# Performance work log

Hardware: AMD Instinct MI355X
Metric: run time of the kernel (lower is better)

## Reference

```python
import jax, jax.numpy as jnp
import numpy as np

B, S, E, H = 4, 2048, 1024, 16
DK = E // H  # 64


def setup_inputs() -> dict:
    key = jax.random.key(0)
    ks = jax.random.split(key, 12)
    sc_in = 1.0 / np.sqrt(E)
    sc_dk = 1.0 / np.sqrt(DK)
    inp = {
        "Q": jax.random.normal(ks[0], (B, S, E), jnp.float32),
        "K": jax.random.normal(ks[1], (B, S, E), jnp.float32),
        "V": jax.random.normal(ks[2], (B, S, E), jnp.float32),
        # per-head projection weights, torch Linear layout [out, in] stacked over heads
        "Wq": jax.random.normal(ks[3], (H, DK, E), jnp.float32) * sc_in,
        "bq": jax.random.normal(ks[4], (H, DK), jnp.float32) * sc_in,
        "Wk": jax.random.normal(ks[5], (H, DK, E), jnp.float32) * sc_in,
        "bk": jax.random.normal(ks[6], (H, DK), jnp.float32) * sc_in,
        "Wv": jax.random.normal(ks[7], (H, DK, E), jnp.float32) * sc_in,
        "bv": jax.random.normal(ks[8], (H, DK), jnp.float32) * sc_in,
        # output projection (intended embed_dim -> embed_dim)
        "Wo": jax.random.normal(ks[9], (E, E), jnp.float32) * sc_in,
        "bo": jax.random.normal(ks[10], (E,), jnp.float32) * sc_in,
    }
    return inp


def reference(Q, K, V, Wq, bq, Wk, bk, Wv, bv, Wo, bo):
    scale = 1.0 / jnp.sqrt(jnp.asarray(DK, Q.dtype))
    # per-head linear projections (vectorized over heads): [B,H,S,DK]
    q = jnp.einsum("bse,hde->bhsd", Q, Wq) + bq[None, :, None, :]
    k = jnp.einsum("bse,hde->bhsd", K, Wk) + bk[None, :, None, :]
    v = jnp.einsum("bse,hde->bhsd", V, Wv) + bv[None, :, None, :]
    # scaled dot-product attention (no mask, dropout=0.0)
    scores = jnp.einsum("bhsd,bhtd->bhst", q, k) * scale  # [B,H,S,S]
    attn = jax.nn.softmax(scores, axis=-1)
    ctx = jnp.einsum("bhst,bhtd->bhsd", attn, v)  # [B,H,S,DK]
    # concat heads along feature dim -> [B,S,E]
    ctx = ctx.transpose(0, 2, 1, 3).reshape(B, S, E)
    return ctx @ Wo.T + bo
```

## Files before the change

kernel.cpp:

```cpp
#include <hip/hip_runtime.h>
#include <stdint.h>

typedef __attribute__((ext_vector_type(8))) short vs8;
typedef __attribute__((ext_vector_type(4))) short vs4;
typedef __attribute__((ext_vector_type(4))) float vf4;

#define DEV static __device__ __forceinline__

DEV unsigned short f2bf(float x){
  union { float f; uint32_t u; } v; v.f = x;
  uint32_t r = v.u + 0x7fffu + ((v.u >> 16) & 1u);
  return (unsigned short)(r >> 16);
}

DEV void gload_lds16(const void* g, void* l){
  __builtin_amdgcn_global_load_lds((const __attribute__((address_space(1))) void*)g,
                                   (__attribute__((address_space(3))) void*)l, 16, 0, 0);
}

DEV int cvtpk(float lo, float hi_){
  int r; asm("v_cvt_pk_bf16_f32 %0, %1, %2" : "=v"(r) : "v"(lo), "v"(hi_)); return r;
}

__global__ void cvt_w(const float* __restrict__ s, unsigned short* __restrict__ d, int n){
  int i = (blockIdx.x * blockDim.x + threadIdx.x) * 4;
  if (i >= n) return;
  vf4 f = *reinterpret_cast<const vf4*>(s + i);
  vs4 o;
  o[0] = (short)f2bf(f[0]); o[1] = (short)f2bf(f[1]);
  o[2] = (short)f2bf(f[2]); o[3] = (short)f2bf(f[3]);
  *reinterpret_cast<vs4*>(d + i) = o;
}


DEV void stage_bf16(const unsigned short* __restrict__ g, long row0, int K, int kt,
                    unsigned short* lds, int lane, int wid){
#pragma unroll
  for (int i = 0; i < 4; ++i){
    int stripe = wid*32 + i*8;
    int row = stripe + (lane >> 3);
    int chunk = (lane & 7) ^ (row & 7);
    const unsigned short* src = g + (row0 + row) * (long)K + kt + chunk*8;
    gload_lds16(src, &lds[stripe*64]);
  }
}

DEV vs8 lds_frag(const unsigned short* lds, int row, int slot){
  return *reinterpret_cast<const vs8*>(&lds[row*64 + (slot ^ (row & 7))*8]);
}

template<int OUT_F32, int BIAS_ROW>
__global__ __launch_bounds__(256)
void gemm_bt(const unsigned short* __restrict__ Ap, const unsigned short* __restrict__ Bp,
             const float* __restrict__ bias, void* __restrict__ Cp,
             int M, int N, int K, float oscale, long aB, long bB, long cB)
{
  __shared__ unsigned short As[128*64];
  __shared__ unsigned short Bs[128*64];
  const int tid = threadIdx.x, lane = tid & 63, wid = tid >> 6;
  const int nt = N >> 7, mt = M >> 7;
  int idx = blockIdx.x;
  const int per = mt * nt;
  const int batch = idx / per; idx -= batch * per;
  const long m0 = (long)(idx / nt) * 128;
  const long n0 = (long)(idx % nt) * 128;
  const int wm = (wid >> 1) * 64, wn = (wid & 1) * 64;
  const int cl = lane & 15, gr = lane >> 4;

  vf4 acc[4][4] = {};

  for (int kt = 0; kt < K; kt += 64){
    stage_bf16(Ap + aB*batch, m0, K, kt, As, lane, wid);
    stage_bf16(Bp + bB*batch, n0, K, kt, Bs, lane, wid);
    __syncthreads();
#pragma unroll
    for (int ks = 0; ks < 2; ++ks){
      vs8 af[4], bf[4];
#pragma unroll
      for (int mi = 0; mi < 4; ++mi) af[mi] = lds_frag(As, wm + mi*16 + cl, ks*4 + gr);
#pragma unroll
      for (int ni = 0; ni < 4; ++ni) bf[ni] = lds_frag(Bs, wn + ni*16 + cl, ks*4 + gr);
#pragma unroll
      for (int mi = 0; mi < 4; ++mi)
#pragma unroll
        for (int ni = 0; ni < 4; ++ni)
          acc[mi][ni] = __builtin_amdgcn_mfma_f32_16x16x32_bf16(af[mi], bf[ni], acc[mi][ni], 0, 0, 0);
    }
    __syncthreads();
  }

#pragma unroll
  for (int mi = 0; mi < 4; ++mi)
#pragma unroll
    for (int ni = 0; ni < 4; ++ni)
#pragma unroll
      for (int r = 0; r < 4; ++r){
        long m = m0 + wm + mi*16 + gr*4 + r;
        long n = n0 + wn + ni*16 + cl;
        float v = (acc[mi][ni][r] + (BIAS_ROW ? bias[m] : bias[n])) * oscale;
        if (OUT_F32) (((float*)Cp) + cB*batch)[m*(long)N + n] = v;
        else (((unsigned short*)Cp) + cB*batch)[m*(long)N + n] = f2bf(v);
      }
}

__global__ __launch_bounds__(256)
void attn_kernel(const unsigned short* __restrict__ qg, const unsigned short* __restrict__ kg,
                 const unsigned short* __restrict__ vg, unsigned short* __restrict__ og)
{
  __shared__ __align__(16) unsigned short Ks[2][64*64];
  __shared__ __align__(16) unsigned short Vs[2][8*64*8];
  __shared__ __align__(16) unsigned short Pl[4][16*72];
  const int tid = threadIdx.x, lane = tid & 63, wid = tid >> 6;
  const int cl = lane & 15, gr = lane >> 4;
  const int bid = blockIdx.x;
  const int qb = bid & 31, h = (bid >> 5) & 15, b = bid >> 9;
  const int s0 = qb*64 + wid*16;

  const unsigned short* qp = qg + ((long)(b*2048 + s0 + cl))*1024 + h*64 + gr*8;
  vs8 q0 = *(const vs8*)(qp);
  vs8 q1 = *(const vs8*)(qp + 32);

  const unsigned short* kb = kg + ((long)b*2048)*1024 + h*64;
  const unsigned short* vb = vg + ((long)(b*1024) + h*64)*2048;

  vf4 o0 = {}, o1 = {}, o2 = {}, o3 = {};
  float m = -__builtin_inff(), lsum = 0.f;

  const int krow = tid >> 3;
  const int kchunk = ((tid & 7) ^ (krow & 7)) * 8;
  const int vd = tid >> 2, vsl = tid & 3;
  const int kbase = (tid & 192) * 8;
  unsigned short* Pw = Pl[wid];

  gload_lds16(kb + (long)krow*1024 + kchunk,        &Ks[0][kbase]);
  gload_lds16(kb + (long)(krow + 32)*1024 + kchunk, &Ks[0][32*64 + kbase]);
  {
    vs8 va = *(const vs8*)(vb + (long)vd*2048 + vsl*8);
    vs8 vb2 = *(const vs8*)(vb + (long)vd*2048 + 32 + vsl*8);
    *(vs8*)(&Vs[0][(vsl*64 + vd)*8]) = va;
    *(vs8*)(&Vs[0][((vsl + 4)*64 + vd)*8]) = vb2;
  }
  __syncthreads();

  int cur = 0;
  for (int j0 = 0; j0 < 2048; j0 += 64){
    const int more = (j0 + 64) < 2048;
    vs8 va, vb2;
    if (more){
      const long nj = j0 + 64;
      gload_lds16(kb + (nj + krow)*1024 + kchunk,      &Ks[cur ^ 1][kbase]);
      gload_lds16(kb + (nj + krow + 32)*1024 + kchunk, &Ks[cur ^ 1][32*64 + kbase]);
      va  = *(const vs8*)(vb + (long)vd*2048 + nj + vsl*8);
      vb2 = *(const vs8*)(vb + (long)vd*2048 + nj + 32 + vsl*8);
    }
    const unsigned short* ksb = Ks[cur];
    const unsigned short* vsb = Vs[cur];

    vf4 s[4];
#pragma unroll
    for (int jt = 0; jt < 4; ++jt){
      vf4 z = {};
      vs8 aA = lds_frag(ksb, jt*16 + cl, gr);
      z = __builtin_amdgcn_mfma_f32_16x16x32_bf16(aA, q0, z, 0, 0, 0);
      vs8 aB = lds_frag(ksb, jt*16 + cl, 4 + gr);
      z = __builtin_amdgcn_mfma_f32_16x16x32_bf16(aB, q1, z, 0, 0, 0);
      s[jt] = z;
    }

    float t0 = fmaxf(fmaxf(s[0][0], s[0][1]), fmaxf(s[0][2], s[0][3]));
    float t1 = fmaxf(fmaxf(s[1][0], s[1][1]), fmaxf(s[1][2], s[1][3]));
    float t2 = fmaxf(fmaxf(s[2][0], s[2][1]), fmaxf(s[2][2], s[2][3]));
    float t3 = fmaxf(fmaxf(s[3][0], s[3][1]), fmaxf(s[3][2], s[3][3]));
    float t = fmaxf(fmaxf(t0, t1), fmaxf(t2, t3));
    t = fmaxf(t, __shfl_xor(t, 16));
    t = fmaxf(t, __shfl_xor(t, 32));

    if (__any(t > m + 8.f)){
      float mn = fmaxf(m, t);
      float al = __builtin_amdgcn_exp2f(m - mn);
      m = mn; lsum *= al;
#pragma unroll
      for (int r = 0; r < 4; ++r){ o0[r] *= al; o1[r] *= al; o2[r] *= al; o3[r] *= al; }
    }

#pragma unroll
    for (int jt = 0; jt < 4; ++jt)
#pragma unroll
      for (int r = 0; r < 4; ++r)
        s[jt][r] = __builtin_amdgcn_exp2f(s[jt][r] - m);
    lsum += (((s[0][0]+s[0][1]) + (s[0][2]+s[0][3])) + ((s[1][0]+s[1][1]) + (s[1][2]+s[1][3])))
          + (((s[2][0]+s[2][1]) + (s[2][2]+s[2][3])) + ((s[3][0]+s[3][1]) + (s[3][2]+s[3][3])));

#pragma unroll
    for (int jt = 0; jt < 4; ++jt){
      int2 w;
      w.x = cvtpk(s[jt][0], s[jt][1]);
      w.y = cvtpk(s[jt][2], s[jt][3]);
      *reinterpret_cast<int2*>(&Pw[cl*72 + jt*16 + gr*4]) = w;
    }
    vs8 pa0 = *reinterpret_cast<const vs8*>(&Pw[cl*72 + gr*8]);
    vs8 pa1 = *reinterpret_cast<const vs8*>(&Pw[cl*72 + 32 + gr*8]);

    o0 = __builtin_amdgcn_mfma_f32_16x16x32_bf16(*(const vs8*)(vsb + (gr*64 +  0 + cl)*8), pa0, o0, 0, 0, 0);
    o1 = __builtin_amdgcn_mfma_f32_16x16x32_bf16(*(const vs8*)(vsb + (gr*64 + 16 + cl)*8), pa0, o1, 0, 0, 0);
    o2 = __builtin_amdgcn_mfma_f32_16x16x32_bf16(*(const vs8*)(vsb + (gr*64 + 32 + cl)*8), pa0, o2, 0, 0, 0);
    o3 = __builtin_amdgcn_mfma_f32_16x16x32_bf16(*(const vs8*)(vsb + (gr*64 + 48 + cl)*8), pa0, o3, 0, 0, 0);
    o0 = __builtin_amdgcn_mfma_f32_16x16x32_bf16(*(const vs8*)(vsb + ((4+gr)*64 +  0 + cl)*8), pa1, o0, 0, 0, 0);
    o1 = __builtin_amdgcn_mfma_f32_16x16x32_bf16(*(const vs8*)(vsb + ((4+gr)*64 + 16 + cl)*8), pa1, o1, 0, 0, 0);
    o2 = __builtin_amdgcn_mfma_f32_16x16x32_bf16(*(const vs8*)(vsb + ((4+gr)*64 + 32 + cl)*8), pa1, o2, 0, 0, 0);
    o3 = __builtin_amdgcn_mfma_f32_16x16x32_bf16(*(const vs8*)(vsb + ((4+gr)*64 + 48 + cl)*8), pa1, o3, 0, 0, 0);

    if (more){
      *(vs8*)(&Vs[cur ^ 1][(vsl*64 + vd)*8]) = va;
      *(vs8*)(&Vs[cur ^ 1][((vsl + 4)*64 + vd)*8]) = vb2;
    }
    __syncthreads();
    cur ^= 1;
  }

  float ls = lsum;
  ls += __shfl_xor(ls, 16);
  ls += __shfl_xor(ls, 32);
  float inv = 1.0f / ls;
  unsigned short* ob = og + ((long)(b*2048 + s0 + cl))*1024 + h*64 + gr*4;
  vs4 w0, w1, w2, w3;
#pragma unroll
  for (int r = 0; r < 4; ++r){
    w0[r] = (short)f2bf(o0[r] * inv);
    w1[r] = (short)f2bf(o1[r] * inv);
    w2[r] = (short)f2bf(o2[r] * inv);
    w3[r] = (short)f2bf(o3[r] * inv);
  }
  *(vs4*)(ob +  0) = w0;
  *(vs4*)(ob + 16) = w1;
  *(vs4*)(ob + 32) = w2;
  *(vs4*)(ob + 48) = w3;
}

extern "C" void kernel_launch(void* const* d_in, const int* in_sizes, int n_in,
                              void* d_out, int out_size, void* d_ws, size_t ws_size,
                              hipStream_t stream)
{
  (void)in_sizes; (void)n_in; (void)out_size; (void)ws_size;
  const float* Q  = (const float*)d_in[0];
  const float* K  = (const float*)d_in[1];
  const float* V  = (const float*)d_in[2];
  const float* bq = (const float*)d_in[4];
  const float* bk = (const float*)d_in[6];
  const float* bv = (const float*)d_in[8];
  const float* bo = (const float*)d_in[10];
  const float* Wq = (const float*)d_in[3];
  const float* Wk = (const float*)d_in[5];
  const float* Wv = (const float*)d_in[7];
  const float* Wo = (const float*)d_in[9];

  unsigned short* q   = (unsigned short*)d_ws;
  unsigned short* k   = q   + (size_t)8*1024*1024;
  unsigned short* vT  = k   + (size_t)8*1024*1024;
  unsigned short* ctx = vT  + (size_t)8*1024*1024;
  unsigned short* wqb = ctx + (size_t)8*1024*1024;
  unsigned short* wkb = wqb + (size_t)1024*1024;
  unsigned short* wvb = wkb + (size_t)1024*1024;
  unsigned short* wob = wvb + (size_t)1024*1024;

  unsigned short* Qb = ctx;
  unsigned short* Kb = (unsigned short*)d_out;
  unsigned short* Vb = Kb + (size_t)8*1024*1024;

  const int WN = 1024*1024;
  const int AN = 4*2048*1024;
  cvt_w<<<1024, 256, 0, stream>>>(Wq, wqb, WN);
  cvt_w<<<1024, 256, 0, stream>>>(Wk, wkb, WN);
  cvt_w<<<1024, 256, 0, stream>>>(Wv, wvb, WN);
  cvt_w<<<1024, 256, 0, stream>>>(Wo, wob, WN);
  cvt_w<<<8192, 256, 0, stream>>>(Q, Qb, AN);
  cvt_w<<<8192, 256, 0, stream>>>(K, Kb, AN);
  cvt_w<<<8192, 256, 0, stream>>>(V, Vb, AN);

  const float qscale = 0.125f * 1.4426950408889634f;

  gemm_bt<0,0><<<512, 256, 0, stream>>>(Qb, wqb, bq, q, 8192, 1024, 1024, qscale, 0, 0, 0);
  gemm_bt<0,0><<<512, 256, 0, stream>>>(Kb, wkb, bk, k, 8192, 1024, 1024, 1.0f, 0, 0, 0);
  gemm_bt<0,1><<<512, 256, 0, stream>>>(wvb, Vb, bv, vT, 1024, 2048, 1024, 1.0f,
                                        0, (long)2048*1024, (long)1024*2048);
  attn_kernel<<<2048, 256, 0, stream>>>(q, k, vT, ctx);
  gemm_bt<1,0><<<512, 256, 0, stream>>>(ctx, wob, bo, d_out, 8192, 1024, 1024, 1.0f, 0, 0, 0);
}
```

Measured before the change: 416.7 us.

## Double-buffer GEMM LDS tiles and widen attention blocks to 128 queries

The projection GEMM now keeps two LDS buffers for A and B, loading the next K tile while MFMAs run on the current one, and needs one barrier per iteration instead of two. The attention kernel now runs 512 threads (8 waves) per block over 128 query rows, so each K/V tile loaded into LDS serves twice as many queries and each thread issues half as many loads. In exchange, GEMM LDS use doubles to 64KB per block, which may reduce occupancy, and the larger attention blocks halve the grid and may also lower occupancy.

```diff
diff --git a/kernel.cpp b/kernel.cpp
--- a/kernel.cpp
+++ b/kernel.cpp
@@ -55,8 +55,8 @@
              const float* __restrict__ bias, void* __restrict__ Cp,
              int M, int N, int K, float oscale, long aB, long bB, long cB)
 {
-  __shared__ unsigned short As[128*64];
-  __shared__ unsigned short Bs[128*64];
+  __shared__ unsigned short As[2][128*64];
+  __shared__ unsigned short Bs[2][128*64];
   const int tid = threadIdx.x, lane = tid & 63, wid = tid >> 6;
   const int nt = N >> 7, mt = M >> 7;
   int idx = blockIdx.x;
@@ -66,20 +66,30 @@
   const long n0 = (long)(idx % nt) * 128;
   const int wm = (wid >> 1) * 64, wn = (wid & 1) * 64;
   const int cl = lane & 15, gr = lane >> 4;
+  const unsigned short* Ab = Ap + aB*batch;
+  const unsigned short* Bb = Bp + bB*batch;
 
   vf4 acc[4][4] = {};
 
+  stage_bf16(Ab, m0, K, 0, As[0], lane, wid);
+  stage_bf16(Bb, n0, K, 0, Bs[0], lane, wid);
+  __syncthreads();
+
+  int cur = 0;
   for (int kt = 0; kt < K; kt += 64){
-    stage_bf16(Ap + aB*batch, m0, K, kt, As, lane, wid);
-    stage_bf16(Bp + bB*batch, n0, K, kt, Bs, lane, wid);
-    __syncthreads();
+    if (kt + 64 < K){
+      stage_bf16(Ab, m0, K, kt + 64, As[cur ^ 1], lane, wid);
+      stage_bf16(Bb, n0, K, kt + 64, Bs[cur ^ 1], lane, wid);
+    }
+    const unsigned short* Asb = As[cur];
+    const unsigned short* Bsb = Bs[cur];
 #pragma unroll
     for (int ks = 0; ks < 2; ++ks){
       vs8 af[4], bf[4];
 #pragma unroll
-      for (int mi = 0; mi < 4; ++mi) af[mi] = lds_frag(As, wm + mi*16 + cl, ks*4 + gr);
-#pragma unroll
-      for (int ni = 0; ni < 4; ++ni) bf[ni] = lds_frag(Bs, wn + ni*16 + cl, ks*4 + gr);
+      for (int mi = 0; mi < 4; ++mi) af[mi] = lds_frag(Asb, wm + mi*16 + cl, ks*4 + gr);
+#pragma unroll
+      for (int ni = 0; ni < 4; ++ni) bf[ni] = lds_frag(Bsb, wn + ni*16 + cl, ks*4 + gr);
 #pragma unroll
       for (int mi = 0; mi < 4; ++mi)
 #pragma unroll
@@ -87,6 +97,7 @@
           acc[mi][ni] = __builtin_amdgcn_mfma_f32_16x16x32_bf16(af[mi], bf[ni], acc[mi][ni], 0, 0, 0);
     }
     __syncthreads();
+    cur ^= 1;
   }
 
 #pragma unroll
@@ -103,18 +114,18 @@
       }
 }
 
-__global__ __launch_bounds__(256)
+__global__ __launch_bounds__(512)
 void attn_kernel(const unsigned short* __restrict__ qg, const unsigned short* __restrict__ kg,
                  const unsigned short* __restrict__ vg, unsigned short* __restrict__ og)
 {
   __shared__ __align__(16) unsigned short Ks[2][64*64];
   __shared__ __align__(16) unsigned short Vs[2][8*64*8];
-  __shared__ __align__(16) unsigned short Pl[4][16*72];
+  __shared__ __align__(16) unsigned short Pl[8][16*72];
   const int tid = threadIdx.x, lane = tid & 63, wid = tid >> 6;
   const int cl = lane & 15, gr = lane >> 4;
   const int bid = blockIdx.x;
-  const int qb = bid & 31, h = (bid >> 5) & 15, b = bid >> 9;
-  const int s0 = qb*64 + wid*16;
+  const int qb = bid & 15, h = (bid >> 4) & 15, b = bid >> 8;
+  const int s0 = qb*128 + wid*16;
 
   const unsigned short* qp = qg + ((long)(b*2048 + s0 + cl))*1024 + h*64 + gr*8;
   vs8 q0 = *(const vs8*)(qp);
@@ -128,30 +139,25 @@
 
   const int krow = tid >> 3;
   const int kchunk = ((tid & 7) ^ (krow & 7)) * 8;
-  const int vd = tid >> 2, vsl = tid & 3;
-  const int kbase = (tid & 192) * 8;
+  const int vd = tid >> 3, vsl = tid & 7;
+  const int kbase = (tid & 448) * 8;
   unsigned short* Pw = Pl[wid];
 
-  gload_lds16(kb + (long)krow*1024 + kchunk,        &Ks[0][kbase]);
-  gload_lds16(kb + (long)(krow + 32)*1024 + kchunk, &Ks[0][32*64 + kbase]);
+  gload_lds16(kb + (long)krow*1024 + kchunk, &Ks[0][kbase]);
   {
     vs8 va = *(const vs8*)(vb + (long)vd*2048 + vsl*8);
-    vs8 vb2 = *(const vs8*)(vb + (long)vd*2048 + 32 + vsl*8);
     *(vs8*)(&Vs[0][(vsl*64 + vd)*8]) = va;
-    *(vs8*)(&Vs[0][((vsl + 4)*64 + vd)*8]) = vb2;
   }
   __syncthreads();
 
   int cur = 0;
   for (int j0 = 0; j0 < 2048; j0 += 64){
     const int more = (j0 + 64) < 2048;
-    vs8 va, vb2;
+    vs8 va;
     if (more){
       const long nj = j0 + 64;
-      gload_lds16(kb + (nj + krow)*1024 + kchunk,      &Ks[cur ^ 1][kbase]);
-      gload_lds16(kb + (nj + krow + 32)*1024 + kchunk, &Ks[cur ^ 1][32*64 + kbase]);
-      va  = *(const vs8*)(vb + (long)vd*2048 + nj + vsl*8);
-      vb2 = *(const vs8*)(vb + (long)vd*2048 + nj + 32 + vsl*8);
+      gload_lds16(kb + (nj + krow)*1024 + kchunk, &Ks[cur ^ 1][kbase]);
+      va = *(const vs8*)(vb + (long)vd*2048 + nj + vsl*8);
     }
     const unsigned short* ksb = Ks[cur];
     const unsigned short* vsb = Vs[cur];
@@ -210,10 +216,8 @@
     o2 = __builtin_amdgcn_mfma_f32_16x16x32_bf16(*(const vs8*)(vsb + ((4+gr)*64 + 32 + cl)*8), pa1, o2, 0, 0, 0);
     o3 = __builtin_amdgcn_mfma_f32_16x16x32_bf16(*(const vs8*)(vsb + ((4+gr)*64 + 48 + cl)*8), pa1, o3, 0, 0, 0);
 
-    if (more){
+    if (more)
       *(vs8*)(&Vs[cur ^ 1][(vsl*64 + vd)*8]) = va;
-      *(vs8*)(&Vs[cur ^ 1][((vsl + 4)*64 + vd)*8]) = vb2;
-    }
     __syncthreads();
     cur ^= 1;
   }
@@ -283,6 +287,6 @@
   gemm_bt<0,0><<<512, 256, 0, stream>>>(Kb, wkb, bk, k, 8192, 1024, 1024, 1.0f, 0, 0, 0);
   gemm_bt<0,1><<<512, 256, 0, stream>>>(wvb, Vb, bv, vT, 1024, 2048, 1024, 1.0f,
                                         0, (long)2048*1024, (long)1024*2048);
-  attn_kernel<<<2048, 256, 0, stream>>>(q, k, vT, ctx);
+  attn_kernel<<<1024, 512, 0, stream>>>(q, k, vT, ctx);
   gemm_bt<1,0><<<512, 256, 0, stream>>>(ctx, wob, bo, d_out, 8192, 1024, 1024, 1.0f, 0, 0, 0);
 }
```

New measurement: 391.3 us. 1.06x faster.
